# Kernel tuning notes

Hardware: AMD Instinct MI355X
Metric: run time of the kernel (lower is better)

The kernel has to match this reference:

```python
import jax, jax.numpy as jnp
import numpy as np

# Dimensions: B rollouts, NTOT nodes, D max out-degree (dense padded adjacency),
# H agent hidden dim, T max_steps (rollout runs T+1 steps incl. stop step).
B, NTOT, D, H, T = 4096, 100000, 32, 64, 8
STOP = -1          # recorded action value for 'stop' (STOP_RELATION)
NEG = -1e9         # mask value for invalid edges
MIN_TEMPERATURE = 1e-5
LN_EPS = 1e-5


def setup_inputs() -> dict:
    key = jax.random.key(0)
    ks = jax.random.split(key, 12)
    q_tokens = jax.random.normal(ks[0], (B, H), dtype=jnp.float32)
    nbr_node = jax.random.randint(ks[1], (NTOT, D), 0, NTOT, dtype=jnp.int32)
    start_nodes = jax.random.randint(ks[2], (B,), 0, NTOT, dtype=jnp.int32)
    edge_valid = jax.random.randint(ks[3], (NTOT, D), 0, 2) == 1
    s = 1.0 / np.sqrt(H)
    action_keys = jax.random.normal(ks[4], (NTOT, D, H), dtype=jnp.float32) * s
    W_init = jax.random.normal(ks[5], (H, H), dtype=jnp.float32) * s
    W_h = jax.random.normal(ks[6], (H, H), dtype=jnp.float32) * s
    W_k = jax.random.normal(ks[7], (H, H), dtype=jnp.float32) * s
    ln_gamma = jnp.ones((H + 2,), jnp.float32)
    ln_beta = jnp.zeros((H + 2,), jnp.float32)
    stop_w = jax.random.normal(ks[8], (H + 2,), dtype=jnp.float32) * 0.1
    stop_b = jnp.zeros((), jnp.float32)
    temperature = jnp.asarray(1.0, jnp.float32)
    return {
        'q_tokens': q_tokens, 'nbr_node': nbr_node, 'start_nodes': start_nodes,
        'edge_valid': edge_valid, 'action_keys': action_keys,
        'W_init': W_init, 'W_h': W_h, 'W_k': W_k,
        'ln_gamma': ln_gamma, 'ln_beta': ln_beta,
        'stop_w': stop_w, 'stop_b': stop_b, 'temperature': temperature,
    }


def _layernorm(x, g, b):
    mu = x.mean(-1, keepdims=True)
    xc = x - mu
    var = (xc * xc).mean(-1, keepdims=True)
    return xc * jax.lax.rsqrt(var + LN_EPS) * g + b


def reference(q_tokens, nbr_node, start_nodes, edge_valid, action_keys,
              W_init, W_h, W_k, ln_gamma, ln_beta, stop_w, stop_b, temperature):
    tclamp = jnp.maximum(temperature, MIN_TEMPERATURE)
    hidden0 = jnp.tanh(q_tokens @ W_init)              # agent.initialize_state
    nB = q_tokens.shape[0]

    def step(carry, t):
        hidden, curr, stopped = carry                  # [nB,H], [nB], [nB]
        keys = action_keys[curr]                       # gather: [nB,D,H]
        horizon = t >= T
        valid = edge_valid[curr] & (~stopped)[:, None] & (~horizon)
        scores = jnp.einsum('bh,bdh->bd', hidden, keys)
        has_edge = valid.any(-1)
        step_frac = jnp.full((nB, 1), t.astype(hidden.dtype) / T)
        stop_in = jnp.concatenate(
            [hidden, step_frac, has_edge[:, None].astype(hidden.dtype)], -1)
        stop_logit = _layernorm(stop_in, ln_gamma, ln_beta) @ stop_w + stop_b
        logits = jnp.concatenate(
            [jnp.where(valid, scores, NEG), stop_logit[:, None]], -1) / tclamp
        logp = jax.nn.log_softmax(logits, -1)
        action = jnp.where(stopped, D, jnp.argmax(logits, -1))
        log_pf = jnp.where(stopped, 0.0,
                           jnp.take_along_axis(logp, action[:, None], 1)[:, 0])
        chose_stop = action == D
        a = jnp.minimum(action, D - 1)
        tails = jnp.take_along_axis(nbr_node[curr], a[:, None], 1)[:, 0]
        sel = jnp.take_along_axis(keys, a[:, None, None], 1)[:, 0, :]
        new_hidden = jnp.tanh(hidden @ W_h + sel @ W_k)  # agent state update
        hidden = jnp.where(chose_stop[:, None], hidden, new_hidden)
        act_rec = jnp.where(chose_stop, STOP,
                            curr.astype(jnp.int32) * D + a.astype(jnp.int32))
        curr = jnp.where(chose_stop, curr, tails)
        stopped = stopped | chose_stop
        return (hidden, curr, stopped), (log_pf, act_rec.astype(jnp.int32))

    init = (hidden0, start_nodes, jnp.zeros((nB,), bool))
    _, (lp, ar) = jax.lax.scan(step, init, jnp.arange(T + 1))
    log_pf_steps = lp.T                                 # [nB, T+1]
    actions_seq = ar.T                                  # [nB, T+1]
    log_pf_total = log_pf_steps.sum(1)
    num_moves = (actions_seq != STOP).sum(1)
    return actions_seq, log_pf_total, log_pf_steps, num_moves
```

## Files before the change

### kernel.cpp

```cpp
#include <hip/hip_runtime.h>
#include <math.h>


namespace {
constexpr int Bx   = 4096;
constexpr int Dx   = 32;
constexpr int Hx   = 64;
constexpr int Tx   = 8;
constexpr float NEGV   = -1e9f;
constexpr float LN_EPS = 1e-5f;
constexpr float MIN_T  = 1e-5f;
}

__device__ __forceinline__ float wave_sum64(float v) {
#pragma unroll
  for (int m = 32; m >= 1; m >>= 1) v += __shfl_xor(v, m);
  return v;
}
__device__ __forceinline__ float wave_max64(float v) {
#pragma unroll
  for (int m = 32; m >= 1; m >>= 1) v = fmaxf(v, __shfl_xor(v, m));
  return v;
}

__global__ __launch_bounds__(256, 4) void gflow_rollout(
    const float* __restrict__ q_tokens,
    const int*   __restrict__ nbr_node,
    const int*   __restrict__ start_nodes,
    const int*   __restrict__ edge_valid,
    const float* __restrict__ action_keys,
    const float* __restrict__ W_init,
    const float* __restrict__ W_h,
    const float* __restrict__ W_k,
    const float* __restrict__ ln_gamma,
    const float* __restrict__ ln_beta,
    const float* __restrict__ stop_w,
    const float* __restrict__ stop_b,
    const float* __restrict__ temperature,
    float* __restrict__ out)
{
  __shared__ float Wh_s[Hx * Hx];
  __shared__ float Wk_s[Hx * Hx];
  __shared__ float h_s[4][Hx];
  __shared__ float sel_s[4][Hx];

  const int tid   = threadIdx.x;
  const int lane  = tid & 63;
  const int wslot = tid >> 6;
  const int b     = blockIdx.x * 4 + wslot;

  {
    const float4* sh = (const float4*)W_h;
    const float4* sk = (const float4*)W_k;
    float4* dh = (float4*)Wh_s;
    float4* dk = (float4*)Wk_s;
#pragma unroll
    for (int i = 0; i < (Hx * Hx / 4) / 256; ++i) {
      dh[tid + i * 256] = sh[tid + i * 256];
      dk[tid + i * 256] = sk[tid + i * 256];
    }
  }

  const float g_j  = ln_gamma[lane];
  const float be_j = ln_beta[lane];
  const float w_j  = stop_w[lane];
  const float g64 = ln_gamma[64], g65 = ln_gamma[65];
  const float b64 = ln_beta[64],  b65 = ln_beta[65];
  const float w64 = stop_w[64],   w65 = stop_w[65];
  const float sb  = stop_b[0];
  const float tcl = fmaxf(temperature[0], MIN_T);

  sel_s[wslot][lane] = q_tokens[b * Hx + lane];
  __syncthreads();
  float acc0 = 0.f;
#pragma unroll 16
  for (int i = 0; i < Hx; ++i)
    acc0 = fmaf(sel_s[wslot][i], W_init[i * Hx + lane], acc0);
  float hid = tanhf(acc0);
  h_s[wslot][lane] = hid;
  __syncthreads();

  int   cur      = start_nodes[b];
  bool  stopped  = false;
  float lp_total = 0.f;
  int   nmoves   = 0;

  const int d    = lane & 31;
  const int half = lane >> 5;

  for (int t = 0; t <= Tx; ++t) {
    float4 kq[8];
    if (!stopped) {
      const float4* kp =
          (const float4*)(action_keys + ((size_t)cur * Dx + d) * Hx + half * 32);
#pragma unroll
      for (int c = 0; c < 8; ++c) kq[c] = kp[c];
    } else {
#pragma unroll
      for (int c = 0; c < 8; ++c) kq[c] = make_float4(0.f, 0.f, 0.f, 0.f);
    }

    float part = 0.f;
    {
      const float* hp = &h_s[wslot][half * 32];
#pragma unroll
      for (int c = 0; c < 8; ++c) {
        float4 hv = *(const float4*)(hp + 4 * c);
        part = fmaf(kq[c].x, hv.x, part);
        part = fmaf(kq[c].y, hv.y, part);
        part = fmaf(kq[c].z, hv.z, part);
        part = fmaf(kq[c].w, hv.w, part);
      }
    }
    const float score = part + __shfl_xor(part, 32);

    const bool horizon = (t == Tx);
    int evi = 0;
    if (!stopped && !horizon) evi = edge_valid[(size_t)cur * Dx + d];
    const bool validd = (evi != 0);
    const unsigned long long vmask = __ballot(validd);
    const bool has_edge = (vmask != 0ULL);

    const float sf = (float)t / (float)Tx;
    const float he = has_edge ? 1.0f : 0.0f;
    float xs = hid;
    if (lane == 0) xs += sf;
    if (lane == 1) xs += he;
    const float mu = wave_sum64(xs) / 66.0f;
    const float dcj = hid - mu;
    float vs = dcj * dcj;
    if (lane == 0) { float dd = sf - mu; vs += dd * dd; }
    if (lane == 1) { float dd = he - mu; vs += dd * dd; }
    const float var  = wave_sum64(vs) / 66.0f;
    const float rstd = rsqrtf(var + LN_EPS);
    float contrib = (dcj * rstd * g_j + be_j) * w_j;
    if (lane == 0) contrib += ((sf - mu) * rstd * g64 + b64) * w64;
    if (lane == 1) contrib += ((he - mu) * rstd * g65 + b65) * w65;
    const float stop_logit = wave_sum64(contrib) + sb;

    float lg;
    if (lane < 32)       lg = (validd ? score : NEGV) / tcl;
    else if (lane == 32) lg = stop_logit / tcl;
    else                 lg = -INFINITY;
    const float mx = wave_max64(lg);
    const float ex = (lane <= 32) ? expf(lg - mx) : 0.f;
    const float se = wave_sum64(ex);

    int action;
    if (stopped) {
      action = Dx;
    } else {
      unsigned long long am = __ballot(lg == mx);
      action = __ffsll((unsigned long long)am) - 1;
    }
    const float lga = __shfl(lg, action & 63);
    const float lp  = stopped ? 0.f : (lga - mx - logf(se));

    const bool chose_stop = (action == Dx);
    const int  a    = min(action, Dx - 1);
    const int  tail = nbr_node[(size_t)cur * Dx + a];

    if (!chose_stop) {
      sel_s[wslot][lane] = action_keys[((size_t)cur * Dx + a) * Hx + lane];
    }
    __syncthreads();

    float a1 = 0.f, a2 = 0.f;
#pragma unroll 8
    for (int i = 0; i < Hx; i += 4) {
      float4 hv = *(const float4*)&h_s[wslot][i];
      float4 sv = *(const float4*)&sel_s[wslot][i];
      a1 = fmaf(hv.x, Wh_s[(i + 0) * Hx + lane], a1);
      a2 = fmaf(sv.x, Wk_s[(i + 0) * Hx + lane], a2);
      a1 = fmaf(hv.y, Wh_s[(i + 1) * Hx + lane], a1);
      a2 = fmaf(sv.y, Wk_s[(i + 1) * Hx + lane], a2);
      a1 = fmaf(hv.z, Wh_s[(i + 2) * Hx + lane], a1);
      a2 = fmaf(sv.z, Wk_s[(i + 2) * Hx + lane], a2);
      a1 = fmaf(hv.w, Wh_s[(i + 3) * Hx + lane], a1);
      a2 = fmaf(sv.w, Wk_s[(i + 3) * Hx + lane], a2);
    }
    const float nh = tanhf(a1 + a2);
    __syncthreads();

    if (!chose_stop) {
      hid = nh;
      h_s[wslot][lane] = hid;
    }
    __syncthreads();

    const int rec = chose_stop ? -1 : (cur * Dx + a);
    if (!chose_stop) { cur = tail; nmoves++; }
    lp_total += lp;
    stopped = stopped || chose_stop;

    if (lane == 0) {
      out[b * (Tx + 1) + t] = (float)rec;
      out[Bx * (Tx + 1) + Bx + b * (Tx + 1) + t] = lp;
    }
  }

  if (lane == 0) {
    out[Bx * (Tx + 1) + b] = lp_total;
    out[Bx * (Tx + 1) + Bx + Bx * (Tx + 1) + b] = (float)nmoves;
  }
}

extern "C" void kernel_launch(void* const* d_in, const int* in_sizes, int n_in,
                              void* d_out, int out_size, void* d_ws, size_t ws_size,
                              hipStream_t stream) {
  const float* q_tokens    = (const float*)d_in[0];
  const int*   nbr_node    = (const int*)d_in[1];
  const int*   start_nodes = (const int*)d_in[2];
  const int*   edge_valid  = (const int*)d_in[3];
  const float* action_keys = (const float*)d_in[4];
  const float* W_init      = (const float*)d_in[5];
  const float* W_h         = (const float*)d_in[6];
  const float* W_k         = (const float*)d_in[7];
  const float* ln_gamma    = (const float*)d_in[8];
  const float* ln_beta     = (const float*)d_in[9];
  const float* stop_w      = (const float*)d_in[10];
  const float* stop_b      = (const float*)d_in[11];
  const float* temperature = (const float*)d_in[12];
  float* out = (float*)d_out;

  dim3 grid(Bx / 4);
  dim3 block(256);
  gflow_rollout<<<grid, block, 0, stream>>>(
      q_tokens, nbr_node, start_nodes, edge_valid, action_keys,
      W_init, W_h, W_k, ln_gamma, ln_beta, stop_w, stop_b, temperature, out);
}
```

Before: 951.7 us.

## Keep rollout state in registers, prefetch next node data, exit early on stop

Removes the per-wave shared buffers for hidden and selected keys and broadcasts values with readlane, which drops the three block-wide barriers per step. The next node's action keys and its edge_valid/nbr_node row are loaded right after the action is chosen, so these gathers overlap the hidden-state matvec. Each wave leaves the loop once it picks stop and fills the remaining steps with padding, and the last step skips the score computation. The cost is more registers for the 32-float key tile plus the readlane-heavy matvecs. Per-wave early exit also depends on there being no barriers left inside the loop.

Measured after the change: 941.3 us. Within noise of the previous version (-1.1%).

```diff
diff --git a/kernel.cpp b/kernel.cpp
--- a/kernel.cpp
+++ b/kernel.cpp
@@ -3,24 +3,27 @@
 
 
 namespace {
-constexpr int Bx   = 4096;
-constexpr int Dx   = 32;
-constexpr int Hx   = 64;
-constexpr int Tx   = 8;
+constexpr int Bx = 4096;
+constexpr int Dx = 32;
+constexpr int Hx = 64;
+constexpr int Tx = 8;
 constexpr float NEGV   = -1e9f;
 constexpr float LN_EPS = 1e-5f;
 constexpr float MIN_T  = 1e-5f;
 }
 
-__device__ __forceinline__ float wave_sum64(float v) {
+__device__ __forceinline__ float wsum(float v) {
 #pragma unroll
   for (int m = 32; m >= 1; m >>= 1) v += __shfl_xor(v, m);
   return v;
 }
-__device__ __forceinline__ float wave_max64(float v) {
+__device__ __forceinline__ float wmax(float v) {
 #pragma unroll
   for (int m = 32; m >= 1; m >>= 1) v = fmaxf(v, __shfl_xor(v, m));
   return v;
+}
+__device__ __forceinline__ float lanebc(float v, int i) {
+  return __int_as_float(__builtin_amdgcn_readlane(__float_as_int(v), i));
 }
 
 __global__ __launch_bounds__(256, 4) void gflow_rollout(
@@ -41,13 +44,25 @@
 {
   __shared__ float Wh_s[Hx * Hx];
   __shared__ float Wk_s[Hx * Hx];
-  __shared__ float h_s[4][Hx];
-  __shared__ float sel_s[4][Hx];
 
   const int tid   = threadIdx.x;
   const int lane  = tid & 63;
   const int wslot = tid >> 6;
   const int b     = blockIdx.x * 4 + wslot;
+  const int d     = lane & 31;
+  const int half  = lane >> 5;
+
+  int cur = start_nodes[b];
+
+  float kf[32];
+  {
+    const float4* kp =
+        (const float4*)(action_keys + ((size_t)cur * Dx + d) * Hx + half * 32);
+#pragma unroll
+    for (int c = 0; c < 8; ++c) ((float4*)kf)[c] = kp[c];
+  }
+  const int* evn_base = (lane < Dx) ? edge_valid : nbr_node;
+  int evnb = evn_base[(size_t)cur * Dx + d];
 
   {
     const float4* sh = (const float4*)W_h;
@@ -55,7 +70,7 @@
     float4* dh = (float4*)Wh_s;
     float4* dk = (float4*)Wk_s;
 #pragma unroll
-    for (int i = 0; i < (Hx * Hx / 4) / 256; ++i) {
+    for (int i = 0; i < 4; ++i) {
       dh[tid + i * 256] = sh[tid + i * 256];
       dk[tid + i * 256] = sk[tid + i * 256];
     }
@@ -70,138 +85,108 @@
   const float sb  = stop_b[0];
   const float tcl = fmaxf(temperature[0], MIN_T);
 
-  sel_s[wslot][lane] = q_tokens[b * Hx + lane];
+  float hid;
+  {
+    const float qv = q_tokens[b * Hx + lane];
+    float acc0 = 0.f;
+#pragma unroll
+    for (int i = 0; i < Hx; ++i)
+      acc0 = fmaf(lanebc(qv, i), W_init[i * Hx + lane], acc0);
+    hid = tanhf(acc0);
+  }
+
   __syncthreads();
-  float acc0 = 0.f;
-#pragma unroll 16
-  for (int i = 0; i < Hx; ++i)
-    acc0 = fmaf(sel_s[wslot][i], W_init[i * Hx + lane], acc0);
-  float hid = tanhf(acc0);
-  h_s[wslot][lane] = hid;
-  __syncthreads();
-
-  int   cur      = start_nodes[b];
-  bool  stopped  = false;
+
   float lp_total = 0.f;
   int   nmoves   = 0;
-
-  const int d    = lane & 31;
-  const int half = lane >> 5;
+  int   tstop    = Tx;
+
+  float* out_act = out + (size_t)b * (Tx + 1);
+  float* out_lps = out + (size_t)Bx * (Tx + 1) + Bx + (size_t)b * (Tx + 1);
 
   for (int t = 0; t <= Tx; ++t) {
-    float4 kq[8];
-    if (!stopped) {
-      const float4* kp =
-          (const float4*)(action_keys + ((size_t)cur * Dx + d) * Hx + half * 32);
-#pragma unroll
-      for (int c = 0; c < 8; ++c) kq[c] = kp[c];
-    } else {
-#pragma unroll
-      for (int c = 0; c < 8; ++c) kq[c] = make_float4(0.f, 0.f, 0.f, 0.f);
-    }
-
-    float part = 0.f;
-    {
-      const float* hp = &h_s[wslot][half * 32];
-#pragma unroll
-      for (int c = 0; c < 8; ++c) {
-        float4 hv = *(const float4*)(hp + 4 * c);
-        part = fmaf(kq[c].x, hv.x, part);
-        part = fmaf(kq[c].y, hv.y, part);
-        part = fmaf(kq[c].z, hv.z, part);
-        part = fmaf(kq[c].w, hv.w, part);
+    float score = 0.f;
+    if (t < Tx) {
+      float part = 0.f;
+#pragma unroll
+      for (int i = 0; i < 32; ++i) {
+        const float hlo = lanebc(hid, i);
+        const float hhi = lanebc(hid, i + 32);
+        const float hv  = half ? hhi : hlo;
+        part = fmaf(kf[i], hv, part);
       }
-    }
-    const float score = part + __shfl_xor(part, 32);
-
-    const bool horizon = (t == Tx);
-    int evi = 0;
-    if (!stopped && !horizon) evi = edge_valid[(size_t)cur * Dx + d];
-    const bool validd = (evi != 0);
-    const unsigned long long vmask = __ballot(validd);
-    const bool has_edge = (vmask != 0ULL);
+      score = part + __shfl_xor(part, 32);
+    }
+
+    const bool validd = (lane < Dx) && (evnb != 0) && (t < Tx);
+    const unsigned long long vm = __ballot(validd);
+    const bool has_edge = (vm != 0ULL);
 
     const float sf = (float)t / (float)Tx;
     const float he = has_edge ? 1.0f : 0.0f;
     float xs = hid;
     if (lane == 0) xs += sf;
     if (lane == 1) xs += he;
-    const float mu = wave_sum64(xs) / 66.0f;
+    const float mu  = wsum(xs) / 66.0f;
     const float dcj = hid - mu;
     float vs = dcj * dcj;
-    if (lane == 0) { float dd = sf - mu; vs += dd * dd; }
-    if (lane == 1) { float dd = he - mu; vs += dd * dd; }
-    const float var  = wave_sum64(vs) / 66.0f;
+    if (lane == 0) { const float dd = sf - mu; vs += dd * dd; }
+    if (lane == 1) { const float dd = he - mu; vs += dd * dd; }
+    const float var  = wsum(vs) / 66.0f;
     const float rstd = rsqrtf(var + LN_EPS);
     float contrib = (dcj * rstd * g_j + be_j) * w_j;
     if (lane == 0) contrib += ((sf - mu) * rstd * g64 + b64) * w64;
     if (lane == 1) contrib += ((he - mu) * rstd * g65 + b65) * w65;
-    const float stop_logit = wave_sum64(contrib) + sb;
+    const float stop_logit = wsum(contrib) + sb;
 
     float lg;
-    if (lane < 32)       lg = (validd ? score : NEGV) / tcl;
-    else if (lane == 32) lg = stop_logit / tcl;
+    if (lane < Dx)       lg = (validd ? score : NEGV) / tcl;
+    else if (lane == Dx) lg = stop_logit / tcl;
     else                 lg = -INFINITY;
-    const float mx = wave_max64(lg);
-    const float ex = (lane <= 32) ? expf(lg - mx) : 0.f;
-    const float se = wave_sum64(ex);
-
-    int action;
-    if (stopped) {
-      action = Dx;
-    } else {
-      unsigned long long am = __ballot(lg == mx);
-      action = __ffsll((unsigned long long)am) - 1;
-    }
-    const float lga = __shfl(lg, action & 63);
-    const float lp  = stopped ? 0.f : (lga - mx - logf(se));
+    const float mx = wmax(lg);
+    const float ex = (lane <= Dx) ? expf(lg - mx) : 0.f;
+    const float se = wsum(ex);
+    const unsigned long long am = __ballot(lg == mx);
+    const int   action = __ffsll(am) - 1;
+    const float lga    = __shfl(lg, action);
+    const float lp     = lga - mx - logf(se);
 
     const bool chose_stop = (action == Dx);
-    const int  a    = min(action, Dx - 1);
-    const int  tail = nbr_node[(size_t)cur * Dx + a];
-
-    if (!chose_stop) {
-      sel_s[wslot][lane] = action_keys[((size_t)cur * Dx + a) * Hx + lane];
-    }
-    __syncthreads();
+    const int  a = min(action, Dx - 1);
+
+    if (lane == 0) {
+      out_act[t] = chose_stop ? -1.0f : (float)(cur * Dx + a);
+      out_lps[t] = lp;
+    }
+    lp_total += lp;
+
+    if (chose_stop) { tstop = t; break; }
+    nmoves++;
+
+    const float selv = action_keys[((size_t)cur * Dx + a) * Hx + lane];
+
+    cur = __shfl(evnb, Dx + a);
+    if (t + 1 < Tx) {
+      const float4* kp =
+          (const float4*)(action_keys + ((size_t)cur * Dx + d) * Hx + half * 32);
+#pragma unroll
+      for (int c = 0; c < 8; ++c) ((float4*)kf)[c] = kp[c];
+      evnb = evn_base[(size_t)cur * Dx + d];
+    }
 
     float a1 = 0.f, a2 = 0.f;
-#pragma unroll 8
-    for (int i = 0; i < Hx; i += 4) {
-      float4 hv = *(const float4*)&h_s[wslot][i];
-      float4 sv = *(const float4*)&sel_s[wslot][i];
-      a1 = fmaf(hv.x, Wh_s[(i + 0) * Hx + lane], a1);
-      a2 = fmaf(sv.x, Wk_s[(i + 0) * Hx + lane], a2);
-      a1 = fmaf(hv.y, Wh_s[(i + 1) * Hx + lane], a1);
-      a2 = fmaf(sv.y, Wk_s[(i + 1) * Hx + lane], a2);
-      a1 = fmaf(hv.z, Wh_s[(i + 2) * Hx + lane], a1);
-      a2 = fmaf(sv.z, Wk_s[(i + 2) * Hx + lane], a2);
-      a1 = fmaf(hv.w, Wh_s[(i + 3) * Hx + lane], a1);
-      a2 = fmaf(sv.w, Wk_s[(i + 3) * Hx + lane], a2);
-    }
-    const float nh = tanhf(a1 + a2);
-    __syncthreads();
-
-    if (!chose_stop) {
-      hid = nh;
-      h_s[wslot][lane] = hid;
-    }
-    __syncthreads();
-
-    const int rec = chose_stop ? -1 : (cur * Dx + a);
-    if (!chose_stop) { cur = tail; nmoves++; }
-    lp_total += lp;
-    stopped = stopped || chose_stop;
-
-    if (lane == 0) {
-      out[b * (Tx + 1) + t] = (float)rec;
-      out[Bx * (Tx + 1) + Bx + b * (Tx + 1) + t] = lp;
-    }
+#pragma unroll
+    for (int i = 0; i < Hx; ++i) {
+      a1 = fmaf(lanebc(hid,  i), Wh_s[i * Hx + lane], a1);
+      a2 = fmaf(lanebc(selv, i), Wk_s[i * Hx + lane], a2);
+    }
+    hid = tanhf(a1 + a2);
   }
 
   if (lane == 0) {
-    out[Bx * (Tx + 1) + b] = lp_total;
-    out[Bx * (Tx + 1) + Bx + Bx * (Tx + 1) + b] = (float)nmoves;
+    for (int t = tstop + 1; t <= Tx; ++t) { out_act[t] = -1.0f; out_lps[t] = 0.f; }
+    out[(size_t)Bx * (Tx + 1) + b] = lp_total;
+    out[(size_t)Bx * (Tx + 1) + Bx + (size_t)Bx * (Tx + 1) + b] = (float)nmoves;
   }
 }
 
@@ -223,9 +208,7 @@
   const float* temperature = (const float*)d_in[12];
   float* out = (float*)d_out;
 
-  dim3 grid(Bx / 4);
-  dim3 block(256);
-  gflow_rollout<<<grid, block, 0, stream>>>(
+  gflow_rollout<<<dim3(Bx / 4), dim3(256), 0, stream>>>(
       q_tokens, nbr_node, start_nodes, edge_valid, action_keys,
       W_init, W_h, W_k, ln_gamma, ln_beta, stop_w, stop_b, temperature, out);
 }
```
